# Kernel tuning notes

Hardware: AMD Instinct MI355X
Metric: run time of the kernel (lower is better)

The kernel has to match this reference:

```python
import jax, jax.numpy as jnp
import numpy as np

INPUT_SIZE = 512
HIDDEN_SIZE = 1024
OUTPUT_SIZE = 512
BATCH = 64
SEQ = 512


def _xavier(key, shape):
    fan_in, fan_out = shape
    bound = np.sqrt(6.0 / (fan_in + fan_out)).astype(np.float32)
    return jax.random.uniform(key, shape, jnp.float32, -bound, bound)


def setup_inputs() -> dict:
    key = jax.random.key(0)
    ks = jax.random.split(key, 7)
    comb = INPUT_SIZE + HIDDEN_SIZE
    return {
        "x": jax.random.normal(ks[0], (BATCH, SEQ, INPUT_SIZE), jnp.float32),
        "W_i": _xavier(ks[1], (comb, HIDDEN_SIZE)),
        "W_f": _xavier(ks[2], (comb, HIDDEN_SIZE)),
        "W_c": _xavier(ks[3], (comb, HIDDEN_SIZE)),
        "W_o": _xavier(ks[4], (comb, HIDDEN_SIZE)),
        "b_i": jnp.zeros((HIDDEN_SIZE,), jnp.float32),
        "b_f": jnp.zeros((HIDDEN_SIZE,), jnp.float32),
        "b_c": jnp.zeros((HIDDEN_SIZE,), jnp.float32),
        "b_o": jnp.zeros((HIDDEN_SIZE,), jnp.float32),
        "fc_w": _xavier(ks[5], (OUTPUT_SIZE, HIDDEN_SIZE)),  # torch Linear weight [out, in]
        "fc_b": jnp.zeros((OUTPUT_SIZE,), jnp.float32),
    }


def reference(x, W_i, W_f, W_c, W_o, b_i, b_f, b_c, b_o, fc_w, fc_b):
    batch = x.shape[0]
    hidden = W_i.shape[1]
    # Fuse the 4 gate weights into one [in+h, 4h] matrix: single GEMM per step.
    W = jnp.concatenate([W_i, W_f, W_c, W_o], axis=1)  # [in+h, 4h]
    b = jnp.concatenate([b_i, b_f, b_c, b_o], axis=0)  # [4h]

    def step(carry, x_t):
        h, c = carry
        combined = jnp.concatenate([x_t, h], axis=1)        # [B, in+h]
        gates = combined @ W + b                            # [B, 4h]
        i_t, f_t, g_t, o_t = jnp.split(gates, 4, axis=1)
        i_t = jax.nn.sigmoid(i_t)
        f_t = jax.nn.sigmoid(f_t)
        g_t = jnp.tanh(g_t)
        o_t = jax.nn.sigmoid(o_t)
        c = f_t * c + i_t * g_t
        h = o_t * jnp.tanh(c)
        return (h, c), None

    h0 = jnp.zeros((batch, hidden), x.dtype)
    c0 = jnp.zeros((batch, hidden), x.dtype)
    (h_T, _), _ = jax.lax.scan(step, (h0, c0), jnp.swapaxes(x, 0, 1))
    return h_T @ fc_w.T + fc_b  # [B, output_size]
```

## Files before the change

### kernel.cpp

```cpp
#include <hip/hip_runtime.h>

typedef unsigned char u8;
typedef unsigned short u16;
typedef unsigned int u32;
typedef unsigned long long u64;
typedef __attribute__((ext_vector_type(4))) int i32x4;
typedef __attribute__((ext_vector_type(4))) float f32x4;

#define SEQ 512

#define OFF_XBQ  0ull
#define OFF_WXQ  33554432ull
#define OFF_WHQ  35651584ull
#define OFF_SCL  39845888ull
#define OFF_SXG  39878656ull
#define OFF_HIMG 40009728ull
#define OFF_TAG  40271872ull
#define OFF_CTL  40305152ull

__device__ inline u16 f2bf(float f) {
  u32 u = __float_as_uint(f);
  return (u16)((u + 0x7fffu + ((u >> 16) & 1u)) >> 16);
}
__device__ inline float bf2f(u16 u) { return __uint_as_float(((u32)u) << 16); }
__device__ inline float sigm(float x) { return 1.f / (1.f + __expf(-x)); }
__device__ inline float tanh_(float x) { return 1.f - 2.f / (1.f + __expf(2.f * x)); }

#define MFMA_I8(a, b, c_) __builtin_amdgcn_mfma_i32_16x16x64_i8(a, b, c_, 0, 0, 0)

__device__ inline u32 ald32(const u32* p) {
  return __hip_atomic_load(p, __ATOMIC_RELAXED, __HIP_MEMORY_SCOPE_AGENT);
}
__device__ inline void ast32(u32* p, u32 v) {
  __hip_atomic_store(p, v, __ATOMIC_RELAXED, __HIP_MEMORY_SCOPE_AGENT);
}
__device__ inline i32x4 ald128(const void* p) {
  union { u64 q[2]; i32x4 v; } u;
  u.q[0] = __hip_atomic_load((const u64*)p, __ATOMIC_RELAXED, __HIP_MEMORY_SCOPE_AGENT);
  u.q[1] = __hip_atomic_load((const u64*)p + 1, __ATOMIC_RELAXED, __HIP_MEMORY_SCOPE_AGENT);
  return u.v;
}
#define VMWAIT0() asm volatile("s_waitcnt vmcnt(0)" ::: "memory")
#define CBAR()    asm volatile("" ::: "memory")

__global__ void pack_xq(const float* __restrict__ x, u8* __restrict__ xbq,
                        float* __restrict__ sxg) {
  __shared__ u8 st[1024];
  const int bid = blockIdx.x;
  const int brow = bid >> 9, tau = bid & 511;
  const int lane = threadIdx.x;
  const float* src = x + ((size_t)bid << 9) + lane * 8;
  float4 a = *(const float4*)src;
  float4 b = *(const float4*)(src + 4);
  float v[8] = {a.x, a.y, a.z, a.w, b.x, b.y, b.z, b.w};
  float m = 0.f;
#pragma unroll
  for (int j = 0; j < 8; ++j) m = fmaxf(m, fabsf(v[j]));
#pragma unroll
  for (int i = 1; i < 64; i <<= 1) m = fmaxf(m, __shfl_xor(m, i));
  m = fmaxf(m, 1e-20f);
  const float s = m * (1.f / 127.f), inv = 127.f / m;
#pragma unroll
  for (int j = 0; j < 8; ++j) {
    float t = v[j] * inv;
    float hi = rintf(t);
    float lo = rintf((t - hi) * 254.f);
    st[lane * 8 + j] = (u8)(signed char)(int)hi;
    st[512 + lane * 8 + j] = (u8)(signed char)(int)lo;
  }
  __syncthreads();
  const int hl = lane >> 5, ks = (lane >> 2) & 7, kg = lane & 3;
  uint4 u = *(const uint4*)&st[hl * 512 + ks * 64 + kg * 16];
  const int c = tau >> 2, tc = tau & 3, g = brow >> 3, rb = brow & 7;
  const int mrow = tc * 8 + rb, mt = mrow >> 4, m15 = mrow & 15;
  *(uint4*)(xbq + (size_t)(((((c * 8 + g) * 2 + hl) * 2 + mt) * 8 + ks) * 64 +
                           kg * 16 + m15) * 16) = u;
  if (lane == 0) sxg[tau * 64 + brow] = s;
}

__global__ void calc_scales(const float* __restrict__ W0, const float* __restrict__ W1,
                            const float* __restrict__ W2, const float* __restrict__ W3,
                            float* __restrict__ scl) {
  const int id = blockIdx.x * 256 + threadIdx.x;
  const int part = id >> 12, q = (id >> 10) & 3, cc = id & 1023;
  const float* Wg = q == 0 ? W0 : q == 1 ? W1 : q == 2 ? W2 : W3;
  const int r0 = part ? 512 : 0, n = part ? 1024 : 512;
  float mx = 1e-8f;
  for (int k = 0; k < n; ++k) mx = fmaxf(mx, fabsf(Wg[(size_t)(r0 + k) * 1024 + cc]));
  scl[id] = mx * (1.f / 127.f);
}

__global__ void pack_whq(const float* __restrict__ W0, const float* __restrict__ W1,
                         const float* __restrict__ W2, const float* __restrict__ W3,
                         const float* __restrict__ scl, u8* __restrict__ whq) {
  const int id = blockIdx.x * 256 + threadIdx.x;
  const int lane = id & 63, ks = (id >> 6) & 15, q = (id >> 10) & 3;
  const int w = (id >> 12) & 1, slot = id >> 13;
  const int hcol = slot * 32 + w * 16 + (lane & 15);
  const float* Wg = q == 0 ? W0 : q == 1 ? W1 : q == 2 ? W2 : W3;
  const int k0 = ks * 64 + (lane >> 4) * 16;
  const float inv_s = 1.f / scl[4096 + q * 1024 + hcol];
  u8 tmp[16];
#pragma unroll
  for (int j = 0; j < 16; ++j) {
    float v = Wg[(size_t)(512 + k0 + j) * 1024 + hcol] * inv_s;
    tmp[j] = (u8)(signed char)(int)rintf(fminf(fmaxf(v, -127.f), 127.f));
  }
  *(uint4*)(whq + (size_t)id * 16) = *(uint4*)tmp;
}

__global__ void pack_wxq(const float* __restrict__ W0, const float* __restrict__ W1,
                         const float* __restrict__ W2, const float* __restrict__ W3,
                         const float* __restrict__ scl, u8* __restrict__ wxq) {
  const int id = blockIdx.x * 256 + threadIdx.x;
  const int lane = id & 63, ks = (id >> 6) & 7, q = (id >> 9) & 3;
  const int w = (id >> 11) & 1, slot = id >> 12;
  const int hcol = slot * 32 + w * 16 + (lane & 15);
  const float* Wg = q == 0 ? W0 : q == 1 ? W1 : q == 2 ? W2 : W3;
  const int k0 = ks * 64 + (lane >> 4) * 16;
  const float inv_s = 1.f / scl[q * 1024 + hcol];
  u8 tmp[16];
#pragma unroll
  for (int j = 0; j < 16; ++j) {
    float v = Wg[(size_t)(k0 + j) * 1024 + hcol] * inv_s;
    tmp[j] = (u8)(signed char)(int)rintf(fminf(fmaxf(v, -127.f), 127.f));
  }
  *(uint4*)(wxq + (size_t)id * 16) = *(uint4*)tmp;
}

__global__ void __launch_bounds__(192, 1) lstm_main(
    char* __restrict__ ws,
    const float* __restrict__ b_i, const float* __restrict__ b_f,
    const float* __restrict__ b_c, const float* __restrict__ b_o,
    const float* __restrict__ fcw, const float* __restrict__ fcb,
    float* __restrict__ out) {
  __shared__ __align__(16) u8 wh[131072];
  __shared__ __align__(16) u16 ring_[8192];
  __shared__ __align__(16) u8 pub_[512];
  __shared__ u32 flg[16];

  const int tid = threadIdx.x;
  const int wid = tid >> 6;
  const int lane = tid & 63;
  const int kgrp = lane >> 4;
  const int l15 = lane & 15;

  u32 xcd;
  asm volatile("s_getreg_b32 %0, hwreg(HW_REG_XCC_ID, 0, 8)" : "=s"(xcd));
  const int g = (int)(xcd & 7);

  if (tid == 0) {
    u32 s = __hip_atomic_fetch_add((u32*)(ws + OFF_CTL) + g * 16, 1u,
                                   __ATOMIC_RELAXED, __HIP_MEMORY_SCOPE_SYSTEM);
    flg[0] = s; flg[1] = 0; flg[2] = 0; flg[3] = 0;
  }
  __syncthreads();
  const int slot = (int)flg[0];
  if (slot >= 32) return;

  u8* himg = (u8*)(ws + OFF_HIMG) + (size_t)g * 32768;
  u32* tags = (u32*)(ws + OFF_TAG) + g * 1024;
  const float* scl = (const float*)(ws + OFF_SCL);

  {
    const u8* src = (const u8*)(ws + OFF_WHQ) + (size_t)slot * 131072;
    for (int i = 0; i < 43; ++i) {
      int u = i * 192 + tid;
      if (u < 8192) *(uint4*)&wh[u * 16] = *(const uint4*)(src + u * 16);
    }
  }
  __syncthreads();

  if (wid == 2) {
    const u8* xq = (const u8*)(ws + OFF_XBQ);
    const u8* wxs = (const u8*)(ws + OFF_WXQ) + (size_t)slot * 65536;
    const float* sxg = (const float*)(ws + OFF_SXG);
    float swx[2][4], bs[2][4];
#pragma unroll
    for (int w2 = 0; w2 < 2; ++w2) {
      const int cwq = slot * 32 + w2 * 16 + l15;
#pragma unroll
      for (int q = 0; q < 4; ++q) swx[w2][q] = scl[q * 1024 + cwq];
      bs[w2][0] = b_i[cwq]; bs[w2][1] = b_f[cwq];
      bs[w2][2] = b_c[cwq]; bs[w2][3] = b_o[cwq];
    }
    for (int c = 0; c < 128; ++c) {
      if (c >= 2) {
        const u32 need = (u32)(4 * c - 4);
        while (((volatile u32*)flg)[2] < need || ((volatile u32*)flg)[3] < need) {}
        CBAR();
      }
      float sxv[2][4];
#pragma unroll
      for (int mt = 0; mt < 2; ++mt)
#pragma unroll
        for (int r = 0; r < 4; ++r)
          sxv[mt][r] = sxg[(c * 4 + mt * 2 + (kgrp >> 1)) * 64 + g * 8 + (kgrp & 1) * 4 + r];
      i32x4 accH[2][2][4], accL[2][2][4];
#pragma unroll
      for (int mt = 0; mt < 2; ++mt)
#pragma unroll
        for (int w2 = 0; w2 < 2; ++w2)
#pragma unroll
          for (int q = 0; q < 4; ++q) {
            accH[mt][w2][q] = (i32x4){0, 0, 0, 0};
            accL[mt][w2][q] = (i32x4){0, 0, 0, 0};
          }
      const u8* xc = xq + (size_t)(c * 8 + g) * 32768;
#pragma unroll 2
      for (int ks = 0; ks < 8; ++ks) {
        i32x4 aH0 = *(const i32x4*)(xc + (size_t)((0 * 2 + 0) * 8 + ks) * 1024 + lane * 16);
        i32x4 aH1 = *(const i32x4*)(xc + (size_t)((0 * 2 + 1) * 8 + ks) * 1024 + lane * 16);
        i32x4 aL0 = *(const i32x4*)(xc + (size_t)((1 * 2 + 0) * 8 + ks) * 1024 + lane * 16);
        i32x4 aL1 = *(const i32x4*)(xc + (size_t)((1 * 2 + 1) * 8 + ks) * 1024 + lane * 16);
#pragma unroll
        for (int w2 = 0; w2 < 2; ++w2)
#pragma unroll
          for (int q = 0; q < 4; ++q) {
            i32x4 b = *(const i32x4*)(wxs + (size_t)(((w2 * 4 + q) * 8 + ks) * 64 + lane) * 16);
            accH[0][w2][q] = MFMA_I8(aH0, b, accH[0][w2][q]);
            accH[1][w2][q] = MFMA_I8(aH1, b, accH[1][w2][q]);
            accL[0][w2][q] = MFMA_I8(aL0, b, accL[0][w2][q]);
            accL[1][w2][q] = MFMA_I8(aL1, b, accL[1][w2][q]);
          }
      }
#pragma unroll
      for (int mt = 0; mt < 2; ++mt)
#pragma unroll
        for (int w2 = 0; w2 < 2; ++w2)
#pragma unroll
          for (int q = 0; q < 4; ++q) {
            u64 pk = 0;
#pragma unroll
            for (int r = 0; r < 4; ++r) {
              float val = sxv[mt][r] * swx[w2][q] *
                          ((float)accH[mt][w2][q][r] + (float)accL[mt][w2][q][r] * (1.f / 254.f)) +
                          bs[w2][q];
              pk |= (u64)f2bf(val) << (16 * r);
            }
            const int tc = mt * 2 + (kgrp >> 1);
            const int cc2 = (w2 * 4 + q) * 16 + l15;
            const int rb0 = (kgrp & 1) * 4;
            *(u64*)&ring_[(((c & 1) * 4 + tc) * 128 + cc2) * 8 + rb0] = pk;
          }
      asm volatile("s_waitcnt lgkmcnt(0)" ::: "memory");
      ((volatile u32*)flg)[1] = (u32)(c + 1);
    }
    return;
  }

  const int w = wid;
  const int col = slot * 32 + w * 16 + l15;
  const int idx = slot * 2 + w;
  float sA[4];
#pragma unroll
  for (int q = 0; q < 4; ++q) sA[q] = scl[4096 + q * 1024 + col] * (1.f / 127.f);

  float cs[4] = {0.f, 0.f, 0.f, 0.f};
  u32* mytag = tags + idx * 16;
  const u32* mypoll = tags + lane * 16;
  const int rbb = (kgrp & 1) * 4;

  for (int t = 1; t <= SEQ; ++t) {
    const int tau = t - 1, ch = tau >> 2, tc = tau & 3, par = tau & 1;
    while (((volatile u32*)flg)[1] <= (u32)ch) {}
    CBAR();
    f32x4 gx[4];
#pragma unroll
    for (int q = 0; q < 4; ++q) {
      u64 pk = *(const u64*)&ring_[(((ch & 1) * 4 + tc) * 128 + (w * 4 + q) * 16 + l15) * 8 + rbb];
      gx[q][0] = bf2f((u16)pk);         gx[q][1] = bf2f((u16)(pk >> 16));
      gx[q][2] = bf2f((u16)(pk >> 32)); gx[q][3] = bf2f((u16)(pk >> 48));
    }
    const u8* ab = himg + par * 16384 + lane * 16;
    u64 rb = __ballot(ald32(mypoll) >= (u32)tau);
    i32x4 A[16];
    i32x4 acc[4];
#pragma unroll
    for (int q = 0; q < 4; ++q) acc[q] = (i32x4){0, 0, 0, 0};
#pragma unroll
    for (int q4 = 0; q4 < 4; ++q4) {
      const u64 need = 0xFFFFull << (q4 * 16);
      while ((rb & need) != need)
        rb = __ballot(ald32(mypoll) >= (u32)tau);
      CBAR();
#pragma unroll
      for (int k4 = 0; k4 < 4; ++k4)
        A[q4 * 4 + k4] = ald128(ab + (size_t)(q4 * 4 + k4) * 1024);
      if (q4 > 0) {
#pragma unroll
        for (int k4 = 0; k4 < 4; ++k4) {
          const int ks = (q4 - 1) * 4 + k4;
#pragma unroll
          for (int q = 0; q < 4; ++q) {
            i32x4 b = *(const i32x4*)&wh[(size_t)(((w * 4 + q) * 16 + ks) * 64 + lane) * 16];
            acc[q] = MFMA_I8(A[ks], b, acc[q]);
          }
        }
      }
    }
#pragma unroll
    for (int k4 = 0; k4 < 4; ++k4) {
      const int ks = 12 + k4;
#pragma unroll
      for (int q = 0; q < 4; ++q) {
        i32x4 b = *(const i32x4*)&wh[(size_t)(((w * 4 + q) * 16 + ks) * 64 + lane) * 16];
        acc[q] = MFMA_I8(A[ks], b, acc[q]);
      }
    }
#pragma unroll
    for (int r = 0; r < 4; ++r) {
      float p[4];
#pragma unroll
      for (int q = 0; q < 4; ++q) {
        float hiF = (float)acc[q][r];
        float loF = (float)__shfl_xor(acc[q][r], 32);
        p[q] = fmaf(sA[q], fmaf(loF, 1.f / 254.f, hiF), gx[q][r]);
      }
      float iv = sigm(p[0]), fv = sigm(p[1]), gv = tanh_(p[2]), ov = sigm(p[3]);
      float cn = fv * cs[r] + iv * gv;
      cs[r] = cn;
      float h = ov * tanh_(cn);
      float hq = h * 127.f;
      float hi = rintf(hq);
      float lo = rintf((hq - hi) * 254.f);
      if (kgrp < 2) {
        const int rr = kgrp * 4 + r;
        pub_[w * 256 + rr * 16 + l15] = (u8)(signed char)(int)hi;
        pub_[w * 256 + (8 + rr) * 16 + l15] = (u8)(signed char)(int)lo;
      }
    }
    asm volatile("s_waitcnt lgkmcnt(0)" ::: "memory");
    if (lane < 16) {
      uint4 v = *(const uint4*)&pub_[w * 256 + lane * 16];
      u8* dst = himg + (size_t)((t & 1) * 16384) +
                (size_t)(((idx >> 2) * 64 + (idx & 3) * 16 + lane) * 16);
      *(uint4*)dst = v;
    }
    VMWAIT0();
    if (lane == 0) ast32(mytag, (u32)t);
    ((volatile u32*)flg)[2 + w] = (u32)t;
  }

  { u32 tv; do { tv = ald32(tags + lane * 16); } while (!__all(tv >= (u32)SEQ)); }
  CBAR();
  {
    const int row = tid >> 4, c16 = tid & 15;
    const int ocol = slot * 16 + c16;
    const float* wr = fcw + (size_t)ocol * 1024;
    float acc = fcb[ocol];
    const float C1 = 1.f / 127.f, C2 = 1.f / 32258.f;
    for (int ks = 0; ks < 16; ++ks) {
#pragma unroll
      for (int kg = 0; kg < 4; ++kg) {
        union { i32x4 v; signed char b[16]; } H, L;
        H.v = ald128(himg + (size_t)((ks * 64 + kg * 16 + row) * 16));
        L.v = ald128(himg + (size_t)((ks * 64 + kg * 16 + 8 + row) * 16));
        const float* wp = wr + ks * 64 + kg * 16;
#pragma unroll
        for (int j = 0; j < 16; ++j)
          acc += ((float)H.b[j] * C1 + (float)L.b[j] * C2) * wp[j];
      }
    }
    out[(size_t)(g * 8 + row) * 512 + ocol] = acc;
  }
}

extern "C" void kernel_launch(void* const* d_in, const int* in_sizes, int n_in,
                              void* d_out, int out_size, void* d_ws, size_t ws_size,
                              hipStream_t stream) {
  const float* x  = (const float*)d_in[0];
  const float* W0 = (const float*)d_in[1];
  const float* W1 = (const float*)d_in[2];
  const float* W2 = (const float*)d_in[3];
  const float* W3 = (const float*)d_in[4];
  const float* bi = (const float*)d_in[5];
  const float* bf = (const float*)d_in[6];
  const float* bc = (const float*)d_in[7];
  const float* bo = (const float*)d_in[8];
  const float* fcw = (const float*)d_in[9];
  const float* fcb = (const float*)d_in[10];
  float* out = (float*)d_out;

  char* ws = (char*)d_ws;
  pack_xq<<<dim3(32768), dim3(64), 0, stream>>>(x, (u8*)(ws + OFF_XBQ),
                                                (float*)(ws + OFF_SXG));
  calc_scales<<<dim3(32), dim3(256), 0, stream>>>(W0, W1, W2, W3, (float*)(ws + OFF_SCL));
  pack_whq<<<dim3(1024), dim3(256), 0, stream>>>(W0, W1, W2, W3,
                                                 (const float*)(ws + OFF_SCL),
                                                 (u8*)(ws + OFF_WHQ));
  pack_wxq<<<dim3(512), dim3(256), 0, stream>>>(W0, W1, W2, W3,
                                                (const float*)(ws + OFF_SCL),
                                                (u8*)(ws + OFF_WXQ));
  hipMemsetAsync(ws + OFF_HIMG, 0, 262144 + 32768 + 1024, stream);
  lstm_main<<<dim3(256), dim3(192), 0, stream>>>(ws, bi, bf, bc, bo, fcw, fcb, out);
}
```

Measured before the change: 2.023 ms.

## Split hidden columns across 64 blocks per XCD with K-split recurrent waves

Each persistent block now owns 16 hidden columns instead of 32, with 64 blocks per XCD and a grid of 512. The two recurrent waves split the K dimension of the h@W_h product instead of the column range, and combine partial int8 accumulators through shared memory. Wave 0 alone applies the gate nonlinearities and publishes h. The aim is to halve the per-step MFMA chain length and the LDS weight footprint per block, so that two blocks can share a CU. The cost is an extra intra-block handoff every step and twice as many producers in the cross-block tag barrier.

```diff
diff --git a/kernel.cpp b/kernel.cpp
--- a/kernel.cpp
+++ b/kernel.cpp
@@ -4,6 +4,7 @@
 typedef unsigned short u16;
 typedef unsigned int u32;
 typedef unsigned long long u64;
+typedef int i32;
 typedef __attribute__((ext_vector_type(4))) int i32x4;
 typedef __attribute__((ext_vector_type(4))) float f32x4;
 
@@ -16,7 +17,7 @@
 #define OFF_SXG  39878656ull
 #define OFF_HIMG 40009728ull
 #define OFF_TAG  40271872ull
-#define OFF_CTL  40305152ull
+#define OFF_CTL  40304640ull
 
 __device__ inline u16 f2bf(float f) {
   u32 u = __float_as_uint(f);
@@ -95,8 +96,8 @@
                          const float* __restrict__ scl, u8* __restrict__ whq) {
   const int id = blockIdx.x * 256 + threadIdx.x;
   const int lane = id & 63, ks = (id >> 6) & 15, q = (id >> 10) & 3;
-  const int w = (id >> 12) & 1, slot = id >> 13;
-  const int hcol = slot * 32 + w * 16 + (lane & 15);
+  const int slot = id >> 12;
+  const int hcol = slot * 16 + (lane & 15);
   const float* Wg = q == 0 ? W0 : q == 1 ? W1 : q == 2 ? W2 : W3;
   const int k0 = ks * 64 + (lane >> 4) * 16;
   const float inv_s = 1.f / scl[4096 + q * 1024 + hcol];
@@ -114,8 +115,8 @@
                          const float* __restrict__ scl, u8* __restrict__ wxq) {
   const int id = blockIdx.x * 256 + threadIdx.x;
   const int lane = id & 63, ks = (id >> 6) & 7, q = (id >> 9) & 3;
-  const int w = (id >> 11) & 1, slot = id >> 12;
-  const int hcol = slot * 32 + w * 16 + (lane & 15);
+  const int slot = id >> 11;
+  const int hcol = slot * 16 + (lane & 15);
   const float* Wg = q == 0 ? W0 : q == 1 ? W1 : q == 2 ? W2 : W3;
   const int k0 = ks * 64 + (lane >> 4) * 16;
   const float inv_s = 1.f / scl[q * 1024 + hcol];
@@ -128,15 +129,16 @@
   *(uint4*)(wxq + (size_t)id * 16) = *(uint4*)tmp;
 }
 
-__global__ void __launch_bounds__(192, 1) lstm_main(
+__global__ void __launch_bounds__(192, 2) lstm_main(
     char* __restrict__ ws,
     const float* __restrict__ b_i, const float* __restrict__ b_f,
     const float* __restrict__ b_c, const float* __restrict__ b_o,
     const float* __restrict__ fcw, const float* __restrict__ fcb,
     float* __restrict__ out) {
-  __shared__ __align__(16) u8 wh[131072];
-  __shared__ __align__(16) u16 ring_[8192];
-  __shared__ __align__(16) u8 pub_[512];
+  __shared__ __align__(16) u8 wh[65536];
+  __shared__ __align__(16) u16 ring_[4096];
+  __shared__ __align__(16) i32 cmb_[1024];
+  __shared__ __align__(16) u8 pub_[256];
   __shared__ u32 flg[16];
 
   const int tid = threadIdx.x;
@@ -152,37 +154,35 @@
   if (tid == 0) {
     u32 s = __hip_atomic_fetch_add((u32*)(ws + OFF_CTL) + g * 16, 1u,
                                    __ATOMIC_RELAXED, __HIP_MEMORY_SCOPE_SYSTEM);
-    flg[0] = s; flg[1] = 0; flg[2] = 0; flg[3] = 0;
+    flg[0] = s; flg[1] = 0; flg[2] = 0; flg[3] = 0; flg[4] = 0;
   }
   __syncthreads();
   const int slot = (int)flg[0];
-  if (slot >= 32) return;
+  if (slot >= 64) return;
 
   u8* himg = (u8*)(ws + OFF_HIMG) + (size_t)g * 32768;
   u32* tags = (u32*)(ws + OFF_TAG) + g * 1024;
   const float* scl = (const float*)(ws + OFF_SCL);
 
   {
-    const u8* src = (const u8*)(ws + OFF_WHQ) + (size_t)slot * 131072;
-    for (int i = 0; i < 43; ++i) {
+    const u8* src = (const u8*)(ws + OFF_WHQ) + (size_t)slot * 65536;
+    for (int i = 0; i < 22; ++i) {
       int u = i * 192 + tid;
-      if (u < 8192) *(uint4*)&wh[u * 16] = *(const uint4*)(src + u * 16);
+      if (u < 4096) *(uint4*)&wh[u * 16] = *(const uint4*)(src + u * 16);
     }
   }
   __syncthreads();
 
   if (wid == 2) {
     const u8* xq = (const u8*)(ws + OFF_XBQ);
-    const u8* wxs = (const u8*)(ws + OFF_WXQ) + (size_t)slot * 65536;
+    const u8* wxs = (const u8*)(ws + OFF_WXQ) + (size_t)slot * 32768;
     const float* sxg = (const float*)(ws + OFF_SXG);
-    float swx[2][4], bs[2][4];
-#pragma unroll
-    for (int w2 = 0; w2 < 2; ++w2) {
-      const int cwq = slot * 32 + w2 * 16 + l15;
-#pragma unroll
-      for (int q = 0; q < 4; ++q) swx[w2][q] = scl[q * 1024 + cwq];
-      bs[w2][0] = b_i[cwq]; bs[w2][1] = b_f[cwq];
-      bs[w2][2] = b_c[cwq]; bs[w2][3] = b_o[cwq];
+    float swx[4], bs[4];
+    {
+      const int cwq = slot * 16 + l15;
+#pragma unroll
+      for (int q = 0; q < 4; ++q) swx[q] = scl[q * 1024 + cwq];
+      bs[0] = b_i[cwq]; bs[1] = b_f[cwq]; bs[2] = b_c[cwq]; bs[3] = b_o[cwq];
     }
     for (int c = 0; c < 128; ++c) {
       if (c >= 2) {
@@ -196,16 +196,14 @@
 #pragma unroll
         for (int r = 0; r < 4; ++r)
           sxv[mt][r] = sxg[(c * 4 + mt * 2 + (kgrp >> 1)) * 64 + g * 8 + (kgrp & 1) * 4 + r];
-      i32x4 accH[2][2][4], accL[2][2][4];
+      i32x4 accH[2][4], accL[2][4];
 #pragma unroll
       for (int mt = 0; mt < 2; ++mt)
 #pragma unroll
-        for (int w2 = 0; w2 < 2; ++w2)
-#pragma unroll
-          for (int q = 0; q < 4; ++q) {
-            accH[mt][w2][q] = (i32x4){0, 0, 0, 0};
-            accL[mt][w2][q] = (i32x4){0, 0, 0, 0};
-          }
+        for (int q = 0; q < 4; ++q) {
+          accH[mt][q] = (i32x4){0, 0, 0, 0};
+          accL[mt][q] = (i32x4){0, 0, 0, 0};
+        }
       const u8* xc = xq + (size_t)(c * 8 + g) * 32768;
 #pragma unroll 2
       for (int ks = 0; ks < 8; ++ks) {
@@ -214,35 +212,31 @@
         i32x4 aL0 = *(const i32x4*)(xc + (size_t)((1 * 2 + 0) * 8 + ks) * 1024 + lane * 16);
         i32x4 aL1 = *(const i32x4*)(xc + (size_t)((1 * 2 + 1) * 8 + ks) * 1024 + lane * 16);
 #pragma unroll
-        for (int w2 = 0; w2 < 2; ++w2)
-#pragma unroll
-          for (int q = 0; q < 4; ++q) {
-            i32x4 b = *(const i32x4*)(wxs + (size_t)(((w2 * 4 + q) * 8 + ks) * 64 + lane) * 16);
-            accH[0][w2][q] = MFMA_I8(aH0, b, accH[0][w2][q]);
-            accH[1][w2][q] = MFMA_I8(aH1, b, accH[1][w2][q]);
-            accL[0][w2][q] = MFMA_I8(aL0, b, accL[0][w2][q]);
-            accL[1][w2][q] = MFMA_I8(aL1, b, accL[1][w2][q]);
+        for (int q = 0; q < 4; ++q) {
+          i32x4 b = *(const i32x4*)(wxs + (size_t)((q * 8 + ks) * 64 + lane) * 16);
+          accH[0][q] = MFMA_I8(aH0, b, accH[0][q]);
+          accH[1][q] = MFMA_I8(aH1, b, accH[1][q]);
+          accL[0][q] = MFMA_I8(aL0, b, accL[0][q]);
+          accL[1][q] = MFMA_I8(aL1, b, accL[1][q]);
+        }
+      }
+#pragma unroll
+      for (int mt = 0; mt < 2; ++mt)
+#pragma unroll
+        for (int q = 0; q < 4; ++q) {
+          u64 pk = 0;
+#pragma unroll
+          for (int r = 0; r < 4; ++r) {
+            float val = sxv[mt][r] * swx[q] *
+                        ((float)accH[mt][q][r] + (float)accL[mt][q][r] * (1.f / 254.f)) +
+                        bs[q];
+            pk |= (u64)f2bf(val) << (16 * r);
           }
-      }
-#pragma unroll
-      for (int mt = 0; mt < 2; ++mt)
-#pragma unroll
-        for (int w2 = 0; w2 < 2; ++w2)
-#pragma unroll
-          for (int q = 0; q < 4; ++q) {
-            u64 pk = 0;
-#pragma unroll
-            for (int r = 0; r < 4; ++r) {
-              float val = sxv[mt][r] * swx[w2][q] *
-                          ((float)accH[mt][w2][q][r] + (float)accL[mt][w2][q][r] * (1.f / 254.f)) +
-                          bs[w2][q];
-              pk |= (u64)f2bf(val) << (16 * r);
-            }
-            const int tc = mt * 2 + (kgrp >> 1);
-            const int cc2 = (w2 * 4 + q) * 16 + l15;
-            const int rb0 = (kgrp & 1) * 4;
-            *(u64*)&ring_[(((c & 1) * 4 + tc) * 128 + cc2) * 8 + rb0] = pk;
-          }
+          const int tc = mt * 2 + (kgrp >> 1);
+          const int cc = q * 16 + l15;
+          const int rb0 = (kgrp & 1) * 4;
+          *(u64*)&ring_[(((c & 1) * 4 + tc) * 64 + cc) * 8 + rb0] = pk;
+        }
       asm volatile("s_waitcnt lgkmcnt(0)" ::: "memory");
       ((volatile u32*)flg)[1] = (u32)(c + 1);
     }
@@ -250,63 +244,83 @@
   }
 
   const int w = wid;
-  const int col = slot * 32 + w * 16 + l15;
-  const int idx = slot * 2 + w;
+  const int col = slot * 16 + l15;
   float sA[4];
 #pragma unroll
   for (int q = 0; q < 4; ++q) sA[q] = scl[4096 + q * 1024 + col] * (1.f / 127.f);
 
   float cs[4] = {0.f, 0.f, 0.f, 0.f};
-  u32* mytag = tags + idx * 16;
+  u32* mytag = tags + slot * 16;
   const u32* mypoll = tags + lane * 16;
   const int rbb = (kgrp & 1) * 4;
 
   for (int t = 1; t <= SEQ; ++t) {
     const int tau = t - 1, ch = tau >> 2, tc = tau & 3, par = tau & 1;
-    while (((volatile u32*)flg)[1] <= (u32)ch) {}
-    CBAR();
     f32x4 gx[4];
-#pragma unroll
-    for (int q = 0; q < 4; ++q) {
-      u64 pk = *(const u64*)&ring_[(((ch & 1) * 4 + tc) * 128 + (w * 4 + q) * 16 + l15) * 8 + rbb];
-      gx[q][0] = bf2f((u16)pk);         gx[q][1] = bf2f((u16)(pk >> 16));
-      gx[q][2] = bf2f((u16)(pk >> 32)); gx[q][3] = bf2f((u16)(pk >> 48));
+    if (w == 0) {
+      while (((volatile u32*)flg)[1] <= (u32)ch) {}
+      CBAR();
+#pragma unroll
+      for (int q = 0; q < 4; ++q) {
+        u64 pk = *(const u64*)&ring_[(((ch & 1) * 4 + tc) * 64 + q * 16 + l15) * 8 + rbb];
+        gx[q][0] = bf2f((u16)pk);         gx[q][1] = bf2f((u16)(pk >> 16));
+        gx[q][2] = bf2f((u16)(pk >> 32)); gx[q][3] = bf2f((u16)(pk >> 48));
+      }
     }
     const u8* ab = himg + par * 16384 + lane * 16;
-    u64 rb = __ballot(ald32(mypoll) >= (u32)tau);
-    i32x4 A[16];
+    u64 rbal = 0;
+    if (tau > 0) rbal = __ballot(ald32(mypoll) >= (u32)tau);
+    i32x4 A[8];
     i32x4 acc[4];
 #pragma unroll
     for (int q = 0; q < 4; ++q) acc[q] = (i32x4){0, 0, 0, 0};
 #pragma unroll
-    for (int q4 = 0; q4 < 4; ++q4) {
-      const u64 need = 0xFFFFull << (q4 * 16);
-      while ((rb & need) != need)
-        rb = __ballot(ald32(mypoll) >= (u32)tau);
-      CBAR();
+    for (int h2 = 0; h2 < 2; ++h2) {
+      if (tau > 0) {
+        const u64 need = 0xFFFFull << ((w * 2 + h2) * 16);
+        while ((rbal & need) != need)
+          rbal = __ballot(ald32(mypoll) >= (u32)tau);
+        CBAR();
+      }
 #pragma unroll
       for (int k4 = 0; k4 < 4; ++k4)
-        A[q4 * 4 + k4] = ald128(ab + (size_t)(q4 * 4 + k4) * 1024);
-      if (q4 > 0) {
+        A[h2 * 4 + k4] = ald128(ab + (size_t)(w * 8 + h2 * 4 + k4) * 1024);
+      if (h2 == 1) {
 #pragma unroll
         for (int k4 = 0; k4 < 4; ++k4) {
-          const int ks = (q4 - 1) * 4 + k4;
+          const int ks = w * 8 + k4;
 #pragma unroll
           for (int q = 0; q < 4; ++q) {
-            i32x4 b = *(const i32x4*)&wh[(size_t)(((w * 4 + q) * 16 + ks) * 64 + lane) * 16];
-            acc[q] = MFMA_I8(A[ks], b, acc[q]);
+            i32x4 b = *(const i32x4*)&wh[(size_t)(((q * 16 + ks) * 64 + lane)) * 16];
+            acc[q] = MFMA_I8(A[k4], b, acc[q]);
           }
         }
       }
     }
 #pragma unroll
     for (int k4 = 0; k4 < 4; ++k4) {
-      const int ks = 12 + k4;
+      const int ks = w * 8 + 4 + k4;
 #pragma unroll
       for (int q = 0; q < 4; ++q) {
-        i32x4 b = *(const i32x4*)&wh[(size_t)(((w * 4 + q) * 16 + ks) * 64 + lane) * 16];
-        acc[q] = MFMA_I8(A[ks], b, acc[q]);
-      }
+        i32x4 b = *(const i32x4*)&wh[(size_t)(((q * 16 + ks) * 64 + lane)) * 16];
+        acc[q] = MFMA_I8(A[4 + k4], b, acc[q]);
+      }
+    }
+    if (w == 1) {
+#pragma unroll
+      for (int q = 0; q < 4; ++q)
+        *((i32x4*)cmb_ + lane * 4 + q) = acc[q];
+      asm volatile("s_waitcnt lgkmcnt(0)" ::: "memory");
+      ((volatile u32*)flg)[4] = (u32)t;
+      ((volatile u32*)flg)[3] = (u32)t;
+      continue;
+    }
+    while (((volatile u32*)flg)[4] < (u32)t) {}
+    CBAR();
+#pragma unroll
+    for (int q = 0; q < 4; ++q) {
+      i32x4 o = *((const i32x4*)cmb_ + lane * 4 + q);
+      acc[q][0] += o[0]; acc[q][1] += o[1]; acc[q][2] += o[2]; acc[q][3] += o[3];
     }
 #pragma unroll
     for (int r = 0; r < 4; ++r) {
@@ -326,27 +340,27 @@
       float lo = rintf((hq - hi) * 254.f);
       if (kgrp < 2) {
         const int rr = kgrp * 4 + r;
-        pub_[w * 256 + rr * 16 + l15] = (u8)(signed char)(int)hi;
-        pub_[w * 256 + (8 + rr) * 16 + l15] = (u8)(signed char)(int)lo;
+        pub_[rr * 16 + l15] = (u8)(signed char)(int)hi;
+        pub_[(8 + rr) * 16 + l15] = (u8)(signed char)(int)lo;
       }
     }
     asm volatile("s_waitcnt lgkmcnt(0)" ::: "memory");
     if (lane < 16) {
-      uint4 v = *(const uint4*)&pub_[w * 256 + lane * 16];
+      uint4 v = *(const uint4*)&pub_[lane * 16];
       u8* dst = himg + (size_t)((t & 1) * 16384) +
-                (size_t)(((idx >> 2) * 64 + (idx & 3) * 16 + lane) * 16);
+                (size_t)(((slot >> 2) * 64 + (slot & 3) * 16 + lane) * 16);
       *(uint4*)dst = v;
     }
     VMWAIT0();
     if (lane == 0) ast32(mytag, (u32)t);
-    ((volatile u32*)flg)[2 + w] = (u32)t;
+    ((volatile u32*)flg)[2] = (u32)t;
   }
 
   { u32 tv; do { tv = ald32(tags + lane * 16); } while (!__all(tv >= (u32)SEQ)); }
   CBAR();
-  {
-    const int row = tid >> 4, c16 = tid & 15;
-    const int ocol = slot * 16 + c16;
+  if (tid < 64) {
+    const int row = tid >> 3, c8 = tid & 7;
+    const int ocol = slot * 8 + c8;
     const float* wr = fcw + (size_t)ocol * 1024;
     float acc = fcb[ocol];
     const float C1 = 1.f / 127.f, C2 = 1.f / 32258.f;
@@ -393,5 +407,5 @@
                                                 (const float*)(ws + OFF_SCL),
                                                 (u8*)(ws + OFF_WXQ));
   hipMemsetAsync(ws + OFF_HIMG, 0, 262144 + 32768 + 1024, stream);
-  lstm_main<<<dim3(256), dim3(192), 0, stream>>>(ws, bi, bf, bc, bo, fcw, fcb, out);
-}
+  lstm_main<<<dim3(512), dim3(192), 0, stream>>>(ws, bi, bf, bc, bo, fcw, fcb, out);
+}
```

Result: slower. 2.578 ms (+27.5%).
